# Performance work log

Hardware: AMD Instinct MI355X
Metric: run time of the kernel (lower is better)

## Reference

```python
import jax, jax.numpy as jnp
import numpy as np

WS = (8, 8)          # window size
NUM_HEADS = 16
C = 512
B_ = 2048            # batch * num_windows
NW = 256             # num_windows per image (mask dim)
N = WS[0] * WS[1]    # tokens per window = 64


def _relative_position_index():
    coords = np.stack(np.meshgrid(np.arange(WS[0]), np.arange(WS[1]), indexing='ij'))  # [2,Wh,Ww]
    flat = coords.reshape(2, -1)                         # [2,N]
    rel = flat[:, :, None] - flat[:, None, :]            # [2,N,N]
    rel = rel.transpose(1, 2, 0).astype(np.int32)        # [N,N,2]
    rel[..., 0] += WS[0] - 1
    rel[..., 1] += WS[1] - 1
    rel[..., 0] *= 2 * WS[1] - 1
    return jnp.asarray(rel.sum(-1))                      # [N,N] in [0, 225)


def setup_inputs() -> dict:
    key = jax.random.key(0)
    ks = jax.random.split(key, 8)
    return {
        'x': jax.random.normal(ks[0], (B_, N, C), jnp.float32),
        'mask': jax.random.normal(ks[1], (NW, N, N), jnp.float32),
        'qkv_w': jax.random.normal(ks[2], (3 * C, C), jnp.float32) * 0.02,
        'q_bias': jax.random.normal(ks[3], (C,), jnp.float32) * 0.02,
        'v_bias': jax.random.normal(ks[4], (C,), jnp.float32) * 0.02,
        'rpb_table': jax.random.normal(ks[5], ((2 * WS[0] - 1) * (2 * WS[1] - 1), NUM_HEADS), jnp.float32) * 0.02,
        'proj_w': jax.random.normal(ks[6], (C, C), jnp.float32) * 0.02,
        'proj_b': jax.random.normal(ks[7], (C,), jnp.float32) * 0.02,
        'rel_index': _relative_position_index(),
    }


def reference(x, mask, qkv_w, q_bias, v_bias, rpb_table, proj_w, proj_b, rel_index):
    Bw, n, c = x.shape
    h = NUM_HEADS
    d = c // h
    # qkv with bias = [q_bias, 0, v_bias]
    qkv_b = jnp.concatenate([q_bias, jnp.zeros_like(v_bias), v_bias])
    qkv = x @ qkv_w.T + qkv_b                               # [B_,N,3C]
    qkv = qkv.reshape(Bw, n, 3, h, d).transpose(2, 0, 3, 1, 4)
    q, k, v = qkv[0], qkv[1], qkv[2]                        # each [B_,h,N,d]
    scale = d ** -0.5
    attn = jnp.einsum('bhnd,bhmd->bhnm', q * scale, k)      # [B_,h,N,N]
    # gathered relative position bias
    rpb = rpb_table[rel_index.reshape(-1)].reshape(n, n, h).transpose(2, 0, 1)  # [h,N,N]
    attn = attn + rpb[None]
    nW = mask.shape[0]
    attn = attn.reshape(Bw // nW, nW, h, n, n) + mask[None, :, None]
    attn = jax.nn.softmax(attn.reshape(Bw, h, n, n), axis=-1)
    out = jnp.einsum('bhnm,bhmd->bhnd', attn, v)            # [B_,h,N,d]
    out = out.transpose(0, 2, 1, 3).reshape(Bw, n, c)
    return out @ proj_w.T + proj_b
```

## Files before the change

### kernel.cpp

```cpp
#include <hip/hip_runtime.h>

typedef short s16x8 __attribute__((ext_vector_type(8)));
typedef float f32x4 __attribute__((ext_vector_type(4)));

__device__ __forceinline__ unsigned short f2bf(float f) {
    unsigned int u = __builtin_bit_cast(unsigned int, f);
    u += 0x7fffu + ((u >> 16) & 1u);
    return (unsigned short)(u >> 16);
}

__device__ __forceinline__ void gload16(const void* g, void* l) {
    __builtin_amdgcn_global_load_lds(
        (const __attribute__((address_space(1))) unsigned int*)g,
        (__attribute__((address_space(3))) unsigned int*)l,
        16, 0, 0);
}

__global__ void cast_bf16_kernel(const float* __restrict__ src,
                                 unsigned short* __restrict__ dst, int n4) {
    int i = blockIdx.x * 256 + threadIdx.x;
    if (i >= n4) return;
    float4 v = ((const float4*)src)[i];
    ushort4 o;
    o.x = f2bf(v.x); o.y = f2bf(v.y); o.z = f2bf(v.z); o.w = f2bf(v.w);
    ((ushort4*)dst)[i] = o;
}

__global__ void rpb_kernel(const float* __restrict__ table,
                           const int* __restrict__ rel,
                           float* __restrict__ rpb) {
    int t = blockIdx.x * 64 + threadIdx.x;
    int idx = rel[t];
#pragma unroll
    for (int h = 0; h < 16; ++h)
        rpb[h * 4096 + t] = table[idx * 16 + h];
}

template <bool SW>
__device__ __forceinline__ void kloop128(const unsigned short* __restrict__ Ab,
                                         const unsigned short* __restrict__ Bb,
                                         unsigned short* Al, unsigned short* Bl,
                                         int t, int wave, int ln, int hk,
                                         int wr, int wc, f32x4 (&acc)[4][4]) {
    const int row = t >> 2, cg = t & 3;
    for (int k0 = 0; k0 < 512; k0 += 32) {
        gload16(Ab + (size_t)row * 512 + k0 + cg * 8, &Al[wave * 512]);
        gload16(Ab + (size_t)(row + 64) * 512 + k0 + cg * 8, &Al[2048 + wave * 512]);
        gload16(Bb + (size_t)row * 512 + k0 + cg * 8, &Bl[wave * 512]);
        gload16(Bb + (size_t)(row + 64) * 512 + k0 + cg * 8, &Bl[2048 + wave * 512]);
        __syncthreads();
        s16x8 af[4], bf[4];
#pragma unroll
        for (int i = 0; i < 4; ++i)
            af[i] = *(const s16x8*)&Al[(wr + i * 16 + ln) * 32 + hk * 8];
#pragma unroll
        for (int j = 0; j < 4; ++j)
            bf[j] = *(const s16x8*)&Bl[(wc + j * 16 + ln) * 32 + hk * 8];
#pragma unroll
        for (int i = 0; i < 4; ++i)
#pragma unroll
            for (int j = 0; j < 4; ++j) {
                if constexpr (SW)
                    acc[j][i] = __builtin_amdgcn_mfma_f32_16x16x32_bf16(bf[j], af[i], acc[j][i], 0, 0, 0);
                else
                    acc[i][j] = __builtin_amdgcn_mfma_f32_16x16x32_bf16(af[i], bf[j], acc[i][j], 0, 0, 0);
            }
        __syncthreads();
    }
}

template <int MODE, int NCOLS>
__global__ __launch_bounds__(256) void gemm_bt(
    const unsigned short* __restrict__ A, const unsigned short* __restrict__ B,
    const float* __restrict__ bq, const float* __restrict__ bv,
    unsigned short* __restrict__ qb, unsigned short* __restrict__ kb,
    unsigned short* __restrict__ vtb,
    const float* __restrict__ pb, float* __restrict__ out) {
    __shared__ __align__(16) unsigned short smem[10240];
    unsigned short* Al = smem;
    unsigned short* Bl = smem + 4096;

    constexpr int NBN = NCOLS / 128;
    const unsigned int cpx = gridDim.x >> 3;
    const unsigned int wg = (blockIdx.x & 7u) * cpx + (blockIdx.x >> 3);
    const int bm = wg / NBN;
    const int bn = wg % NBN;
    const int t = threadIdx.x;
    const int wave = t >> 6, lane = t & 63;
    const int ln = lane & 15, hk = lane >> 4;
    const int wr = (wave >> 1) * 64, wc = (wave & 1) * 64;

    const f32x4 zero = {0.f, 0.f, 0.f, 0.f};
    f32x4 acc[4][4];
#pragma unroll
    for (int i = 0; i < 4; ++i)
#pragma unroll
        for (int j = 0; j < 4; ++j) acc[i][j] = zero;

    const unsigned short* Ab = A + (size_t)bm * 128 * 512;
    const unsigned short* Bb = B + (size_t)bn * 128 * 512;

    if constexpr (MODE == 1) {
        kloop128<true>(Ab, Bb, Al, Bl, t, wave, ln, hk, wr, wc, acc);
        float* epf = (float*)smem + wave * 1280;
#pragma unroll
        for (int j = 0; j < 4; ++j) {
            const int nn0 = bn * 128 + wc + j * 16 + hk * 4;
            const float4 b4 = *(const float4*)&pb[nn0];
#pragma unroll
            for (int i = 0; i < 4; ++i) {
                const int tk = i * 16 + ln;
                float4 o4;
                o4.x = acc[j][i][0] + b4.x;
                o4.y = acc[j][i][1] + b4.y;
                o4.z = acc[j][i][2] + b4.z;
                o4.w = acc[j][i][3] + b4.w;
                *(float4*)&epf[tk * 20 + hk * 4] = o4;
            }
            const int nnb = bn * 128 + wc + j * 16;
#pragma unroll
            for (int rr = 0; rr < 4; ++rr) {
                const int li = rr * 64 + lane;
                const int tk = li >> 2, c4 = (li & 3) * 4;
                float4 v4 = *(const float4*)&epf[tk * 20 + c4];
                *(float4*)(out + (size_t)(bm * 128 + wr + tk) * NCOLS + nnb + c4) = v4;
            }
        }
    } else {
        const int which = bn >> 2;
        const int bb = bm * 2;
        const size_t winbase = (size_t)((bb + (wr >> 6)) * 16);
        unsigned short* ep = smem + wave * 2560;
        if (which < 2) {
            kloop128<true>(Ab, Bb, Al, Bl, t, wave, ln, hk, wr, wc, acc);
            unsigned short* dst0 = (which == 0) ? qb : kb;
#pragma unroll
            for (int H = 0; H < 2; ++H) {
#pragma unroll
                for (int j2 = 0; j2 < 2; ++j2) {
                    const int j = H * 2 + j2;
                    const int rem0 = (bn * 128 + wc + j * 16 + hk * 4) & 511;
                    float4 b4 = {0.f, 0.f, 0.f, 0.f};
                    if (which == 0) b4 = *(const float4*)&bq[rem0];
                    const int ch0 = j2 * 16 + hk * 4;
#pragma unroll
                    for (int i = 0; i < 4; ++i) {
                        const int tk = i * 16 + ln;
                        ushort4 pk;
                        pk.x = f2bf(acc[j][i][0] + b4.x);
                        pk.y = f2bf(acc[j][i][1] + b4.y);
                        pk.z = f2bf(acc[j][i][2] + b4.z);
                        pk.w = f2bf(acc[j][i][3] + b4.w);
                        *(ushort4*)&ep[tk * 40 + ch0] = pk;
                    }
                }
                const int remH = (bn * 128 + wc + H * 32) & 511;
                const size_t Dq = (winbase + (remH >> 5)) * 2048;
#pragma unroll
                for (int rr = 0; rr < 4; ++rr) {
                    const int li = rr * 64 + lane;
                    const int tk = li >> 2, c8 = (li & 3) * 8;
                    s16x8 val = *(const s16x8*)&ep[tk * 40 + c8];
                    *(s16x8*)(dst0 + Dq + tk * 32 + c8) = val;
                }
            }
        } else {
            kloop128<false>(Ab, Bb, Al, Bl, t, wave, ln, hk, wr, wc, acc);
#pragma unroll
            for (int H = 0; H < 2; ++H) {
#pragma unroll
                for (int j2 = 0; j2 < 2; ++j2) {
                    const int j = H * 2 + j2;
                    const int rem = (bn * 128 + wc + j * 16 + ln) & 511;
                    const float bias = bv[rem];
                    const int ch = j2 * 16 + ln;
#pragma unroll
                    for (int i = 0; i < 4; ++i) {
                        const int tk = i * 16 + hk * 4;
                        ushort4 pk;
                        pk.x = f2bf(acc[i][j][0] + bias);
                        pk.y = f2bf(acc[i][j][1] + bias);
                        pk.z = f2bf(acc[i][j][2] + bias);
                        pk.w = f2bf(acc[i][j][3] + bias);
                        *(ushort4*)&ep[ch * 72 + tk] = pk;
                    }
                }
                const int remH = (bn * 128 + wc + H * 32) & 511;
                const size_t Dv = (winbase + (remH >> 5)) * 2048;
#pragma unroll
                for (int rr = 0; rr < 4; ++rr) {
                    const int li = rr * 64 + lane;
                    const int dd = li >> 3, t8 = (li & 7) * 8;
                    s16x8 val = *(const s16x8*)&ep[dd * 72 + t8];
                    *(s16x8*)(vtb + Dv + dd * 64 + t8) = val;
                }
            }
        }
    }
}

__global__ __launch_bounds__(256) void attn_kernel(
    const unsigned short* __restrict__ qbuf, const unsigned short* __restrict__ kbuf,
    const unsigned short* __restrict__ vtbuf, const float* __restrict__ rpb,
    const float* __restrict__ mask, unsigned short* __restrict__ aout) {
    __shared__ __align__(16) unsigned short ql[64 * 32];
    __shared__ __align__(16) unsigned short kl[64 * 32];
    __shared__ __align__(16) unsigned short vl[32 * 64];
    __shared__ __align__(16) unsigned short plds[64 * 72];

    const int bh = blockIdx.x;
    const int b = bh >> 4, head = bh & 15;
    const int wmask = b & 255;
    const int t = threadIdx.x, wave = t >> 6, lane = t & 63;
    const int ln = lane & 15, hk = lane >> 4;

    const size_t base = (size_t)bh * 2048;
    gload16(qbuf + base + t * 8, &ql[wave * 512]);
    gload16(kbuf + base + t * 8, &kl[wave * 512]);
    gload16(vtbuf + base + t * 8, &vl[wave * 512]);
    __syncthreads();

    const f32x4 zero = {0.f, 0.f, 0.f, 0.f};
    s16x8 aq = *(const s16x8*)&ql[(wave * 16 + ln) * 32 + hk * 8];
    f32x4 sc[4];
#pragma unroll
    for (int j = 0; j < 4; ++j) {
        s16x8 bk = *(const s16x8*)&kl[(j * 16 + ln) * 32 + hk * 8];
        sc[j] = __builtin_amdgcn_mfma_f32_16x16x32_bf16(aq, bk, zero, 0, 0, 0);
    }

    const float scale = 0.17677669529663687f;
    const float* rpb_h = rpb + head * 4096;
    const float* msk = mask + wmask * 4096;

    float p[4][4];
#pragma unroll
    for (int r = 0; r < 4; ++r) {
        const int i = wave * 16 + hk * 4 + r;
        float v[4], m = -1e30f;
#pragma unroll
        for (int j = 0; j < 4; ++j) {
            const int c = j * 16 + ln;
            v[j] = sc[j][r] * scale + rpb_h[i * 64 + c] + msk[i * 64 + c];
            m = fmaxf(m, v[j]);
        }
        for (int off = 1; off < 16; off <<= 1) m = fmaxf(m, __shfl_xor(m, off));
        float s = 0.f;
#pragma unroll
        for (int j = 0; j < 4; ++j) { v[j] = __expf(v[j] - m); s += v[j]; }
        for (int off = 1; off < 16; off <<= 1) s += __shfl_xor(s, off);
        const float inv = 1.f / s;
#pragma unroll
        for (int j = 0; j < 4; ++j) p[r][j] = v[j] * inv;
    }
#pragma unroll
    for (int r = 0; r < 4; ++r)
#pragma unroll
        for (int j = 0; j < 4; ++j)
            plds[(wave * 16 + hk * 4 + r) * 72 + j * 16 + ln] = f2bf(p[r][j]);

    f32x4 o2[2] = {zero, zero};
#pragma unroll
    for (int kt = 0; kt < 2; ++kt) {
        s16x8 ap = *(const s16x8*)&plds[(wave * 16 + ln) * 72 + kt * 32 + hk * 8];
#pragma unroll
        for (int nt = 0; nt < 2; ++nt) {
            s16x8 bvf = *(const s16x8*)&vl[(nt * 16 + ln) * 64 + kt * 32 + hk * 8];
            o2[nt] = __builtin_amdgcn_mfma_f32_16x16x32_bf16(bvf, ap, o2[nt], 0, 0, 0);
        }
    }
    unsigned short* ep = plds + wave * 1152;
#pragma unroll
    for (int nt = 0; nt < 2; ++nt) {
        ushort4 pk;
        pk.x = f2bf(o2[nt][0]); pk.y = f2bf(o2[nt][1]);
        pk.z = f2bf(o2[nt][2]); pk.w = f2bf(o2[nt][3]);
        *(ushort4*)&ep[ln * 40 + nt * 16 + hk * 4] = pk;
    }
    const int tk = lane >> 2, c8 = (lane & 3) * 8;
    s16x8 val = *(const s16x8*)&ep[tk * 40 + c8];
    *(s16x8*)(aout + ((size_t)(b * 64 + wave * 16 + tk)) * 512 + head * 32 + c8) = val;
}

extern "C" void kernel_launch(void* const* d_in, const int* in_sizes, int n_in,
                              void* d_out, int out_size, void* d_ws, size_t ws_size,
                              hipStream_t stream) {
    const float* x      = (const float*)d_in[0];
    const float* mask   = (const float*)d_in[1];
    const float* qkv_w  = (const float*)d_in[2];
    const float* q_bias = (const float*)d_in[3];
    const float* v_bias = (const float*)d_in[4];
    const float* rpb_t  = (const float*)d_in[5];
    const float* proj_w = (const float*)d_in[6];
    const float* proj_b = (const float*)d_in[7];
    const int*   rel    = (const int*)d_in[8];
    float* out = (float*)d_out;

    char* ws = (char*)d_ws;
    unsigned short* xbf   = (unsigned short*)ws;
    unsigned short* qbuf  = (unsigned short*)(ws + 0x08000000);
    unsigned short* kbuf  = (unsigned short*)(ws + 0x10000000);
    unsigned short* vtbuf = (unsigned short*)(ws + 0x18000000);
    unsigned short* wqkv  = (unsigned short*)(ws + 0x20000000);
    unsigned short* wproj = (unsigned short*)(ws + 0x20180000);
    float*          rpb   = (float*)(ws + 0x20200000);
    unsigned short* aout  = xbf;

    cast_bf16_kernel<<<65536, 256, 0, stream>>>(x, xbf, 16777216);
    cast_bf16_kernel<<<768, 256, 0, stream>>>(qkv_w, wqkv, 196608);
    cast_bf16_kernel<<<256, 256, 0, stream>>>(proj_w, wproj, 65536);
    rpb_kernel<<<64, 64, 0, stream>>>(rpb_t, rel, rpb);

    gemm_bt<0, 1536><<<1024 * 12, 256, 0, stream>>>(
        xbf, wqkv, q_bias, v_bias, qbuf, kbuf, vtbuf, nullptr, nullptr);

    attn_kernel<<<32768, 256, 0, stream>>>(qbuf, kbuf, vtbuf, rpb, mask, aout);

    gemm_bt<1, 512><<<1024 * 4, 256, 0, stream>>>(
        aout, wproj, nullptr, nullptr, nullptr, nullptr, nullptr, proj_b, out);
}
```

Baseline: 1.061 ms.

## Double-buffer LDS tiles in GEMM k-loop to overlap loads with MFMA

Splits the GEMM k-loop into two LDS buffers so the global-to-LDS load for the next 32-wide k slice is issued before the MFMAs on the current slice. This halves the number of barriers per k slice and is meant to hide global load latency behind matrix math in both the QKV and projection GEMMs. LDS use per block grows from 20 KB to 32 KB, which may reduce how many blocks fit on a CU.

```diff
diff --git a/kernel.cpp b/kernel.cpp
--- a/kernel.cpp
+++ b/kernel.cpp
@@ -36,35 +36,60 @@
         rpb[h * 4096 + t] = table[idx * 16 + h];
 }
 
+__device__ __forceinline__ void stage_step(const unsigned short* __restrict__ Ab,
+                                           const unsigned short* __restrict__ Bb,
+                                           unsigned short* base, int wave,
+                                           size_t gA0, size_t gA1, int k0) {
+    gload16(Ab + gA0 + k0, &base[wave * 512]);
+    gload16(Ab + gA1 + k0, &base[2048 + wave * 512]);
+    gload16(Bb + gA0 + k0, &base[4096 + wave * 512]);
+    gload16(Bb + gA1 + k0, &base[6144 + wave * 512]);
+}
+
+template <bool SW>
+__device__ __forceinline__ void mfma_step(const unsigned short* base, int ln, int hk,
+                                          int wr, int wc, f32x4 (&acc)[4][4]) {
+    const unsigned short* Al = base;
+    const unsigned short* Bl = base + 4096;
+    s16x8 af[4], bf[4];
+#pragma unroll
+    for (int i = 0; i < 4; ++i)
+        af[i] = *(const s16x8*)&Al[(wr + i * 16 + ln) * 32 + hk * 8];
+#pragma unroll
+    for (int j = 0; j < 4; ++j)
+        bf[j] = *(const s16x8*)&Bl[(wc + j * 16 + ln) * 32 + hk * 8];
+#pragma unroll
+    for (int i = 0; i < 4; ++i)
+#pragma unroll
+        for (int j = 0; j < 4; ++j) {
+            if constexpr (SW)
+                acc[j][i] = __builtin_amdgcn_mfma_f32_16x16x32_bf16(bf[j], af[i], acc[j][i], 0, 0, 0);
+            else
+                acc[i][j] = __builtin_amdgcn_mfma_f32_16x16x32_bf16(af[i], bf[j], acc[i][j], 0, 0, 0);
+        }
+}
+
 template <bool SW>
 __device__ __forceinline__ void kloop128(const unsigned short* __restrict__ Ab,
                                          const unsigned short* __restrict__ Bb,
-                                         unsigned short* Al, unsigned short* Bl,
+                                         unsigned short* smem,
                                          int t, int wave, int ln, int hk,
                                          int wr, int wc, f32x4 (&acc)[4][4]) {
     const int row = t >> 2, cg = t & 3;
-    for (int k0 = 0; k0 < 512; k0 += 32) {
-        gload16(Ab + (size_t)row * 512 + k0 + cg * 8, &Al[wave * 512]);
-        gload16(Ab + (size_t)(row + 64) * 512 + k0 + cg * 8, &Al[2048 + wave * 512]);
-        gload16(Bb + (size_t)row * 512 + k0 + cg * 8, &Bl[wave * 512]);
-        gload16(Bb + (size_t)(row + 64) * 512 + k0 + cg * 8, &Bl[2048 + wave * 512]);
+    const size_t gA0 = (size_t)row * 512 + cg * 8;
+    const size_t gA1 = (size_t)(row + 64) * 512 + cg * 8;
+    unsigned short* b0 = smem;
+    unsigned short* b1 = smem + 8192;
+
+    stage_step(Ab, Bb, b0, wave, gA0, gA1, 0);
+    __syncthreads();
+    for (int k0 = 0; k0 < 512; k0 += 64) {
+        stage_step(Ab, Bb, b1, wave, gA0, gA1, k0 + 32);
+        mfma_step<SW>(b0, ln, hk, wr, wc, acc);
         __syncthreads();
-        s16x8 af[4], bf[4];
-#pragma unroll
-        for (int i = 0; i < 4; ++i)
-            af[i] = *(const s16x8*)&Al[(wr + i * 16 + ln) * 32 + hk * 8];
-#pragma unroll
-        for (int j = 0; j < 4; ++j)
-            bf[j] = *(const s16x8*)&Bl[(wc + j * 16 + ln) * 32 + hk * 8];
-#pragma unroll
-        for (int i = 0; i < 4; ++i)
-#pragma unroll
-            for (int j = 0; j < 4; ++j) {
-                if constexpr (SW)
-                    acc[j][i] = __builtin_amdgcn_mfma_f32_16x16x32_bf16(bf[j], af[i], acc[j][i], 0, 0, 0);
-                else
-                    acc[i][j] = __builtin_amdgcn_mfma_f32_16x16x32_bf16(af[i], bf[j], acc[i][j], 0, 0, 0);
-            }
+        if (k0 + 64 < 512)
+            stage_step(Ab, Bb, b0, wave, gA0, gA1, k0 + 64);
+        mfma_step<SW>(b1, ln, hk, wr, wc, acc);
         __syncthreads();
     }
 }
@@ -76,9 +101,7 @@
     unsigned short* __restrict__ qb, unsigned short* __restrict__ kb,
     unsigned short* __restrict__ vtb,
     const float* __restrict__ pb, float* __restrict__ out) {
-    __shared__ __align__(16) unsigned short smem[10240];
-    unsigned short* Al = smem;
-    unsigned short* Bl = smem + 4096;
+    __shared__ __align__(16) unsigned short smem[16384];
 
     constexpr int NBN = NCOLS / 128;
     const unsigned int cpx = gridDim.x >> 3;
@@ -101,7 +124,7 @@
     const unsigned short* Bb = B + (size_t)bn * 128 * 512;
 
     if constexpr (MODE == 1) {
-        kloop128<true>(Ab, Bb, Al, Bl, t, wave, ln, hk, wr, wc, acc);
+        kloop128<true>(Ab, Bb, smem, t, wave, ln, hk, wr, wc, acc);
         float* epf = (float*)smem + wave * 1280;
 #pragma unroll
         for (int j = 0; j < 4; ++j) {
@@ -132,7 +155,7 @@
         const size_t winbase = (size_t)((bb + (wr >> 6)) * 16);
         unsigned short* ep = smem + wave * 2560;
         if (which < 2) {
-            kloop128<true>(Ab, Bb, Al, Bl, t, wave, ln, hk, wr, wc, acc);
+            kloop128<true>(Ab, Bb, smem, t, wave, ln, hk, wr, wc, acc);
             unsigned short* dst0 = (which == 0) ? qb : kb;
 #pragma unroll
             for (int H = 0; H < 2; ++H) {
@@ -165,7 +188,7 @@
                 }
             }
         } else {
-            kloop128<false>(Ab, Bb, Al, Bl, t, wave, ln, hk, wr, wc, acc);
+            kloop128<false>(Ab, Bb, smem, t, wave, ln, hk, wr, wc, acc);
 #pragma unroll
             for (int H = 0; H < 2; ++H) {
 #pragma unroll
```

Result: faster. 1.012 ms (-4.6%).
